# Kernel optimization log

Hardware: AMD Instinct MI355X
Metric: run time of the kernel (lower is better)

Reference implementation:

```python
import jax, jax.numpy as jnp
import numpy as np

B, T, D = 2, 2048, 1024
HD = 128          # head_dim
NH = 16           # num_attention_heads
NKV = 8           # num_key_value_heads
EPS = 1e-6
ROPE_THETA = 1000000.0


def setup_inputs() -> dict:
    key = jax.random.key(0)
    ks = jax.random.split(key, 7)
    s = 0.02
    return {
        "x": jax.random.normal(ks[0], (B, T, D), dtype=jnp.float32),
        "wq": jax.random.normal(ks[1], (D, NH * HD), dtype=jnp.float32) * s,
        "wk": jax.random.normal(ks[2], (D, NKV * HD), dtype=jnp.float32) * s,
        "wv": jax.random.normal(ks[3], (D, NKV * HD), dtype=jnp.float32) * s,
        "wo": jax.random.normal(ks[4], (NH * HD, D), dtype=jnp.float32) * s,
        "q_norm_w": jnp.ones((HD,), dtype=jnp.float32),
        "k_norm_w": jnp.ones((HD,), dtype=jnp.float32),
    }


def _rms_norm(x, w):
    # torch source: x / (rms + eps) * w  (eps added OUTSIDE the sqrt)
    rms = jnp.sqrt(jnp.mean(x * x, axis=-1, keepdims=True))
    return w * (x / (rms + EPS))


def _rope_cos_sin(seq_len):
    pos = jnp.arange(seq_len, dtype=jnp.float32)
    thetas = ROPE_THETA ** (-2.0 * jnp.arange(HD // 2, dtype=jnp.float32) / HD)
    freqs = pos[:, None] * thetas[None, :]            # [T, HD//2]
    return jnp.cos(freqs), jnp.sin(freqs)


def _apply_rope(x, cos, sin):
    # x: [B, H, T, HD]; interleaved complex pairs (view_as_complex layout)
    xr = x[..., 0::2]
    xi = x[..., 1::2]
    c = cos[None, None, :, :]
    s = sin[None, None, :, :]
    out_r = xr * c - xi * s
    out_i = xr * s + xi * c
    return jnp.stack([out_r, out_i], axis=-1).reshape(x.shape)


def reference(x, wq, wk, wv, wo, q_norm_w, k_norm_w):
    b, t, d = x.shape
    q = (x @ wq).reshape(b, t, NH, HD).transpose(0, 2, 1, 3)    # [B,NH,T,HD]
    k = (x @ wk).reshape(b, t, NKV, HD).transpose(0, 2, 1, 3)   # [B,NKV,T,HD]
    v = (x @ wv).reshape(b, t, NKV, HD).transpose(0, 2, 1, 3)

    q = _rms_norm(q, q_norm_w)
    k = _rms_norm(k, k_norm_w)

    rep = NH // NKV
    k = jnp.repeat(k, rep, axis=1)   # GQA expand -> [B,NH,T,HD]
    v = jnp.repeat(v, rep, axis=1)

    cos, sin = _rope_cos_sin(t)
    q = _apply_rope(q, cos, sin)
    k = _apply_rope(k, cos, sin)

    scale = 1.0 / jnp.sqrt(jnp.float32(HD))
    scores = jnp.einsum("bhqd,bhkd->bhqk", q, k) * scale        # [B,NH,T,T]
    mask = jnp.triu(jnp.full((t, t), -jnp.inf, dtype=scores.dtype), k=1)
    scores = scores + mask
    attn = jax.nn.softmax(scores.astype(jnp.float32), axis=-1).astype(q.dtype)
    y = jnp.einsum("bhqk,bhkd->bhqd", attn, v)                  # [B,NH,T,HD]
    y = y.transpose(0, 2, 1, 3).reshape(b, t, NH * HD)
    return y @ wo
```

## Files before the change

### kernel.cpp

```cpp
#include <hip/hip_runtime.h>
#include <hip/hip_bf16.h>
#include <cstdint>
#include <cstddef>

using bf16 = __hip_bfloat16;
using short8 = __attribute__((ext_vector_type(8))) short;
using f32x4  = __attribute__((ext_vector_type(4))) float;
using f32x16 = __attribute__((ext_vector_type(16))) float;

#define DEVI __device__ __forceinline__

DEVI void async_ld16(const void* g, void* l) {
  __builtin_amdgcn_global_load_lds(
      (const __attribute__((address_space(1))) unsigned int*)g,
      (__attribute__((address_space(3))) unsigned int*)l, 16, 0, 0);
}

DEVI unsigned int cvt_pk_bf16(float lo, float hi) {
  unsigned int r;
  asm("v_cvt_pk_bf16_f32 %0, %1, %2" : "=v"(r) : "v"(lo), "v"(hi));
  return r;
}

__global__ __launch_bounds__(256) void prep(
    const float* __restrict__ x, const float* __restrict__ wq,
    const float* __restrict__ wk, const float* __restrict__ wv,
    const float* __restrict__ wo, bf16* __restrict__ xb,
    bf16* __restrict__ wt, bf16* __restrict__ wot, float2* __restrict__ tab) {
  const int z = blockIdx.x, tid = threadIdx.x;
  if (z < 4096) {
    int i = z * 256 + tid;
    float4 v = ((const float4*)x)[i];
    union { bf16 h[4]; ushort4 u; } o;
    o.h[0] = __float2bfloat16(v.x);
    o.h[1] = __float2bfloat16(v.y);
    o.h[2] = __float2bfloat16(v.z);
    o.h[3] = __float2bfloat16(v.w);
    ((ushort4*)xb)[i] = o.u;
  } else if (z < 10240) {
    __shared__ float tile[32][33];
    const float* src; bf16* dst; int N, K, n0, k0, roff;
    if (z < 8192) {
      int z2 = z - 4096;
      int xb_ = z2 & 31, yb = (z2 >> 5) & 31, zz = z2 >> 10;
      if (zz < 2)       { src = wq; N = 2048; n0 = zz * 1024 + xb_ * 32; roff = zz * 1024 + xb_ * 32; }
      else if (zz == 2) { src = wk; N = 1024; n0 = xb_ * 32; roff = 2048 + xb_ * 32; }
      else              { src = wv; N = 1024; n0 = xb_ * 32; roff = 3072 + xb_ * 32; }
      K = 1024; k0 = yb * 32; dst = wt;
    } else {
      int z3 = z - 8192;
      int xb_ = z3 & 31, yb = z3 >> 5;
      src = wo; N = 1024; K = 2048; n0 = xb_ * 32; k0 = yb * 32; roff = xb_ * 32;
      dst = wot;
    }
    int tx = tid & 31, ty = tid >> 5;
#pragma unroll
    for (int i = 0; i < 32; i += 8)
      tile[ty + i][tx] = src[(size_t)(k0 + ty + i) * N + n0 + tx];
    __syncthreads();
#pragma unroll
    for (int i = 0; i < 32; i += 8)
      dst[(size_t)(roff + ty + i) * K + k0 + tx] = __float2bfloat16(tile[tx][ty + i]);
  } else {
    int z4 = z - 10240;
    int t = z4 * 4 + (tid >> 6), i = tid & 63;
    float ex = -2.f * (float)i * (1.f / 128.f);
    float theta = exp2f(ex * 19.9315685693241741f);
    float f = (float)t * theta;
    float sv, cv;
    sincosf(f, &sv, &cv);
    tab[t * 64 + i] = make_float2(cv, sv);
  }
}

__global__ __launch_bounds__(256, 2) void gemm_qkv(
    const bf16* __restrict__ A, const bf16* __restrict__ Bt,
    const float* __restrict__ qnw, const float* __restrict__ knw,
    const float2* __restrict__ tab,
    bf16* __restrict__ Qh, bf16* __restrict__ Kh, bf16* __restrict__ Vt) {
  __shared__ alignas(16) bf16 As[2][128 * 64];
  __shared__ alignas(16) bf16 Bs[2][128 * 64];
  const int tid = threadIdx.x, lane = tid & 63, w = tid >> 6;
  const int wm = w >> 1, wn = w & 1;
  const int bx = blockIdx.x;
  const int m0 = blockIdx.y * 128, n0 = bx * 128;
  const int K = 1024, nt = 16;
  f32x4 acc[4][4] = {};

  const int srow = lane >> 3;
  const int scb  = (lane & 7) * 16;

  auto stage = [&](int buf, int kt) {
#pragma unroll
    for (int i = 0; i < 4; i++) {
      int row = w * 32 + i * 8 + srow;
      int src_cb = scb ^ ((row & 7) << 4);
      async_ld16((const char*)(A  + (size_t)(m0 + row) * K + kt * 64) + src_cb,
                 (char*)As[buf] + w * 4096 + i * 1024);
      async_ld16((const char*)(Bt + (size_t)(n0 + row) * K + kt * 64) + src_cb,
                 (char*)Bs[buf] + w * 4096 + i * 1024);
    }
  };

  stage(0, 0);
  stage(1, 1);

  for (int kt = 0; kt < nt; ++kt) {
    const int buf = kt & 1;
    if (kt + 1 < nt) asm volatile("s_waitcnt vmcnt(8)" ::: "memory");
    else             asm volatile("s_waitcnt vmcnt(0)" ::: "memory");
    __builtin_amdgcn_s_barrier();
#pragma unroll
    for (int ks = 0; ks < 2; ks++) {
      short8 af[4], bfr[4];
#pragma unroll
      for (int mi = 0; mi < 4; mi++) {
        int row = wm * 64 + mi * 16 + (lane & 15);
        int cb = (ks * 64 + (lane >> 4) * 16) ^ ((row & 7) << 4);
        af[mi] = *(const short8*)((const char*)As[buf] + row * 128 + cb);
      }
#pragma unroll
      for (int ni = 0; ni < 4; ni++) {
        int row = wn * 64 + ni * 16 + (lane & 15);
        int cb = (ks * 64 + (lane >> 4) * 16) ^ ((row & 7) << 4);
        bfr[ni] = *(const short8*)((const char*)Bs[buf] + row * 128 + cb);
      }
#pragma unroll
      for (int mi = 0; mi < 4; mi++)
#pragma unroll
        for (int ni = 0; ni < 4; ni++)
          acc[mi][ni] = __builtin_amdgcn_mfma_f32_16x16x32_bf16(af[mi], bfr[ni], acc[mi][ni], 0, 0, 0);
    }
    __builtin_amdgcn_s_barrier();
    __builtin_amdgcn_sched_barrier(0);
    if (kt + 2 < nt) stage(buf, kt + 2);
  }

  const int b = m0 >> 11;

  if (bx < 24) {
    __syncthreads();
    float* ssb = (float*)As;
    float s[4][4];
#pragma unroll
    for (int mi = 0; mi < 4; mi++)
#pragma unroll
      for (int r = 0; r < 4; r++) {
        float v0 = acc[mi][0][r], v1 = acc[mi][1][r];
        float v2 = acc[mi][2][r], v3 = acc[mi][3][r];
        float t = v0 * v0 + v1 * v1 + v2 * v2 + v3 * v3;
        t += __shfl_xor(t, 1);
        t += __shfl_xor(t, 2);
        t += __shfl_xor(t, 4);
        t += __shfl_xor(t, 8);
        s[mi][r] = t;
      }
    if ((lane & 15) == 0) {
#pragma unroll
      for (int mi = 0; mi < 4; mi++)
#pragma unroll
        for (int r = 0; r < 4; r++)
          ssb[wn * 128 + wm * 64 + mi * 16 + (lane >> 4) * 4 + r] = s[mi][r];
    }
    __syncthreads();

    const int isQ = (bx < 16);
    const int h = isQ ? bx : bx - 16;
    const float* wnp = isQ ? qnw : knw;
    bf16* dst = isQ ? Qh : Kh;
    const int NHH = isQ ? 16 : 8;
    const float qs = isQ ? 0.12751744416163417f : 1.f;
    float wd[4];
#pragma unroll
    for (int ni = 0; ni < 4; ni++) wd[ni] = wnp[wn * 64 + ni * 16 + (lane & 15)];

#pragma unroll
    for (int mi = 0; mi < 4; mi++)
#pragma unroll
      for (int r = 0; r < 4; r++) {
        int rl = wm * 64 + mi * 16 + (lane >> 4) * 4 + r;
        float tot = ssb[rl] + ssb[128 + rl];
        float inv = qs / (sqrtf(tot * 0.0078125f) + 1e-6f);
        int t = (m0 + rl) & 2047;
        bf16* drow = dst + ((size_t)(b * NHH + h) * 2048 + t) * 128;
#pragma unroll
        for (int ni = 0; ni < 4; ni++) {
          int d = wn * 64 + ni * 16 + (lane & 15);
          float val = acc[mi][ni][r] * inv * wd[ni];
          float prt = __shfl_xor(val, 1);
          float2 cs = tab[t * 64 + (d >> 1)];
          float o = (d & 1) ? (prt * cs.y + val * cs.x)
                            : (val * cs.x - prt * cs.y);
          drow[d] = __float2bfloat16(o);
        }
      }
  } else {
    __syncthreads();
    bf16* vt = (bf16*)As;
    const int vh = bx - 24;
#pragma unroll
    for (int mi = 0; mi < 4; mi++)
#pragma unroll
      for (int ni = 0; ni < 4; ni++) {
        int d = wn * 64 + ni * 16 + (lane & 15);
        int tl = wm * 64 + mi * 16 + (lane >> 4) * 4;
        unsigned int p0 = cvt_pk_bf16(acc[mi][ni][0], acc[mi][ni][1]);
        unsigned int p1 = cvt_pk_bf16(acc[mi][ni][2], acc[mi][ni][3]);
        int byte = d * 256 + ((tl * 2) ^ ((d & 7) << 4));
        *(uint2*)((char*)vt + byte) = make_uint2(p0, p1);
      }
    __syncthreads();
    bf16* dstV = Vt + (size_t)(b * 8 + vh) * 128 * 2048 + (m0 & 2047);
#pragma unroll
    for (int i = 0; i < 8; i++) {
      int flat = tid + i * 256;
      int d = flat >> 4, g = flat & 15;
      short8 v = *(const short8*)((const char*)vt + d * 256 + ((g * 16) ^ ((d & 7) << 4)));
      *(short8*)(dstV + (size_t)d * 2048 + g * 8) = v;
    }
  }
}

__global__ __launch_bounds__(256, 3) void gemm_out64(
    const bf16* __restrict__ A, const bf16* __restrict__ Bt,
    float* __restrict__ C, int M, int N, int K) {
  __shared__ alignas(16) bf16 As[2][64 * 64];
  __shared__ alignas(16) bf16 Bs[2][128 * 64];
  const int tid = threadIdx.x, lane = tid & 63, w = tid >> 6;
  const int m0 = blockIdx.y * 64, n0 = blockIdx.x * 128;
  const int nt = K >> 6;
  f32x4 acc[4][2] = {};

  auto stage = [&](int buf, int kt) {
#pragma unroll
    for (int i = 0; i < 2; i++) {
      int c = tid + i * 256;
      int row = c >> 3;
      int cb = ((c & 7) * 16) ^ ((row & 7) << 4);
      async_ld16((const char*)(A + (size_t)(m0 + row) * K + kt * 64) + cb,
                 (char*)As[buf] + i * 4096 + tid * 16);
    }
#pragma unroll
    for (int i = 0; i < 4; i++) {
      int c = tid + i * 256;
      int row = c >> 3;
      int cb = ((c & 7) * 16) ^ ((row & 7) << 4);
      async_ld16((const char*)(Bt + (size_t)(n0 + row) * K + kt * 64) + cb,
                 (char*)Bs[buf] + i * 4096 + tid * 16);
    }
  };

  stage(0, 0);
  stage(1, 1);

  for (int kt = 0; kt < nt; ++kt) {
    const int buf = kt & 1;
    if (kt + 1 < nt) asm volatile("s_waitcnt vmcnt(6)" ::: "memory");
    else             asm volatile("s_waitcnt vmcnt(0)" ::: "memory");
    __builtin_amdgcn_s_barrier();
#pragma unroll
    for (int ks = 0; ks < 2; ks++) {
      short8 af[4], bfr[2];
#pragma unroll
      for (int mi = 0; mi < 4; mi++) {
        int row = mi * 16 + (lane & 15);
        int cb = (ks * 64 + (lane >> 4) * 16) ^ ((row & 7) << 4);
        af[mi] = *(const short8*)((const char*)As[buf] + row * 128 + cb);
      }
#pragma unroll
      for (int ni = 0; ni < 2; ni++) {
        int row = w * 32 + ni * 16 + (lane & 15);
        int cb = (ks * 64 + (lane >> 4) * 16) ^ ((row & 7) << 4);
        bfr[ni] = *(const short8*)((const char*)Bs[buf] + row * 128 + cb);
      }
#pragma unroll
      for (int mi = 0; mi < 4; mi++)
#pragma unroll
        for (int ni = 0; ni < 2; ni++)
          acc[mi][ni] = __builtin_amdgcn_mfma_f32_16x16x32_bf16(af[mi], bfr[ni], acc[mi][ni], 0, 0, 0);
    }
    __builtin_amdgcn_s_barrier();
    __builtin_amdgcn_sched_barrier(0);
    if (kt + 2 < nt) stage(buf, kt + 2);
  }

  const int c0 = n0 + w * 32 + (lane & 15);
  const int r0 = m0 + (lane >> 4) * 4;
#pragma unroll
  for (int mi = 0; mi < 4; mi++)
#pragma unroll
    for (int ni = 0; ni < 2; ni++)
#pragma unroll
      for (int r = 0; r < 4; r++)
        C[(size_t)(r0 + mi * 16 + r) * N + (c0 + ni * 16)] = acc[mi][ni][r];
}

__global__ __launch_bounds__(512, 1) void flash_attn10(
    const bf16* __restrict__ Qh, const bf16* __restrict__ Kh,
    const bf16* __restrict__ Vt, bf16* __restrict__ Y) {
  __shared__ alignas(16) bf16 KB[4][64 * 128];
  __shared__ alignas(16) bf16 VB[4][128 * 64];
  __shared__ float MLs[128][2];
  const int tid = threadIdx.x, lane = tid & 63, w = tid >> 6;
  const int hi = lane >> 5, lq = lane & 31;
  const int grp = w >> 2, wl = w & 3;

  const int g = blockIdx.x;
  const int bh = (g & 7) * 4 + ((g >> 3) & 3);
  const int p  = g >> 5;
  const int b = bh >> 4, h = bh & 15, kvh = h >> 1;

  const bf16* Qg = Qh + (size_t)(b * 16 + h) * 2048 * 128;
  const bf16* Kg = Kh + (size_t)(b * 8 + kvh) * 2048 * 128;
  const bf16* Vg = Vt + (size_t)(b * 8 + kvh) * 128 * 2048;

  short8 qf[8];
  f32x16 oacc[4];
  float m, l;
  int qw = 0, qg = 0;

  auto stage2 = [&](int set, int k0e) {
#pragma unroll
    for (int gb = 0; gb < 2; gb++) {
      const int k0 = k0e + gb * 64;
      char* kb = (char*)KB[set * 2 + gb];
      char* vb = (char*)VB[set * 2 + gb];
#pragma unroll
      for (int i = 0; i < 2; i++) {
        int c = w * 2 + i;
        {
          int row = c * 4 + (lane >> 4);
          int cb = ((lane & 15) * 16) ^ ((row & 7) << 4);
          async_ld16((const char*)Kg + (size_t)(k0 + row) * 256 + cb, kb + c * 1024);
        }
        {
          int row = c * 8 + (lane >> 3);
          int cb = ((lane & 7) * 16) ^ ((row & 7) << 4);
          async_ld16((const char*)Vg + (size_t)row * 4096 + (size_t)k0 * 2 + cb, vb + c * 1024);
        }
      }
    }
  };

  auto setupTile = [&](int q0) {
    qw = q0 + wl * 32;
    qg = qw + lq;
#pragma unroll
    for (int dc = 0; dc < 8; dc++)
      qf[dc] = *(const short8*)(Qg + (size_t)qg * 128 + dc * 16 + hi * 8);
#pragma unroll
    for (int dc = 0; dc < 4; dc++)
#pragma unroll
      for (int r = 0; r < 16; r++) oacc[dc][r] = 0.f;
    m = -1e30f;
    l = 0.f;
  };

  auto computeStep = [&](int bufI, int k0) {
    f32x16 st[2] = {};
#pragma unroll
    for (int kc = 0; kc < 2; kc++) {
      int row = kc * 32 + lq;
      int swz = (row & 7) << 4;
      const char* kbase = (const char*)KB[bufI] + row * 256;
#pragma unroll
      for (int dc = 0; dc < 8; dc++) {
        short8 kf = *(const short8*)(kbase + ((dc * 32 + hi * 16) ^ swz));
        st[kc] = __builtin_amdgcn_mfma_f32_32x32x16_bf16(kf, qf[dc], st[kc], 0, 0, 0);
      }
    }
    const bool msk = (k0 + 63 > qw);
    if (msk) {
#pragma unroll
      for (int kc = 0; kc < 2; kc++)
#pragma unroll
        for (int rr = 0; rr < 16; rr++) {
          int kg = k0 + kc * 32 + (rr & 3) + 8 * (rr >> 2) + 4 * hi;
          if (kg > qg) st[kc][rr] = -1e30f;
        }
    }
    float mx[16];
#pragma unroll
    for (int rr = 0; rr < 16; rr++) mx[rr] = fmaxf(st[0][rr], st[1][rr]);
#pragma unroll
    for (int off = 8; off >= 1; off >>= 1)
#pragma unroll
      for (int rr = 0; rr < 8; rr++)
        if (rr < off) mx[rr] = fmaxf(mx[rr], mx[rr + off]);
    float pm = fmaxf(mx[0], __shfl_xor(mx[0], 32));
    if (__any(pm > m + 8.f)) {
      float mnew = fmaxf(m, pm);
      float alpha = exp2f(m - mnew);
      m = mnew;
      l *= alpha;
      float al[16];
#pragma unroll
      for (int rr = 0; rr < 16; rr++)
        al[rr] = __shfl(alpha, (rr & 3) + 8 * (rr >> 2) + 4 * hi);
#pragma unroll
      for (int dc = 0; dc < 4; dc++)
#pragma unroll
        for (int rr = 0; rr < 16; rr++) oacc[dc][rr] *= al[rr];
    }
#pragma unroll
    for (int kc = 0; kc < 2; kc++)
#pragma unroll
      for (int rr = 0; rr < 16; rr++) st[kc][rr] = exp2f(st[kc][rr] - m);
    float sm[16];
#pragma unroll
    for (int rr = 0; rr < 16; rr++) sm[rr] = st[0][rr] + st[1][rr];
#pragma unroll
    for (int off = 8; off >= 1; off >>= 1)
#pragma unroll
      for (int rr = 0; rr < 8; rr++)
        if (rr < off) sm[rr] += sm[rr + off];
    l += sm[0] + __shfl_xor(sm[0], 32);
    short8 af[4];
#pragma unroll
    for (int kc = 0; kc < 2; kc++)
#pragma unroll
      for (int sb = 0; sb < 2; sb++) {
        int base = sb * 8;
        unsigned int a01 = cvt_pk_bf16(st[kc][base + 0], st[kc][base + 1]);
        unsigned int a23 = cvt_pk_bf16(st[kc][base + 2], st[kc][base + 3]);
        unsigned int b01 = cvt_pk_bf16(st[kc][base + 4], st[kc][base + 5]);
        unsigned int b23 = cvt_pk_bf16(st[kc][base + 6], st[kc][base + 7]);
        unsigned int xa01 = (unsigned int)__shfl_xor((int)a01, 32);
        unsigned int xa23 = (unsigned int)__shfl_xor((int)a23, 32);
        unsigned int xb01 = (unsigned int)__shfl_xor((int)b01, 32);
        unsigned int xb23 = (unsigned int)__shfl_xor((int)b23, 32);
        union { unsigned int u[4]; short8 s; } f;
        f.u[0] = hi ? xb01 : a01;
        f.u[1] = hi ? xb23 : a23;
        f.u[2] = hi ? b01 : xa01;
        f.u[3] = hi ? b23 : xa23;
        af[kc * 2 + sb] = f.s;
      }
#pragma unroll
    for (int dc = 0; dc < 4; dc++) {
      int row = dc * 32 + lq;
      int swz = (row & 7) << 4;
      const char* vbase = (const char*)VB[bufI] + row * 128;
#pragma unroll
      for (int ks = 0; ks < 4; ks++) {
        short8 vf = *(const short8*)(vbase + ((ks * 32 + hi * 16) ^ swz));
        oacc[dc] = __builtin_amdgcn_mfma_f32_32x32x16_bf16(af[ks], vf, oacc[dc], 0, 0, 0);
      }
    }
  };

  auto runRounds = [&](int n) {
    const int R = n >> 1;
    for (int r = 0; r < R; ++r) {
      asm volatile("s_waitcnt vmcnt(0)" ::: "memory");
      __builtin_amdgcn_s_barrier();
      if (r + 1 < R) stage2((r + 1) & 1, (2 * r + 2) * 64);
      __builtin_amdgcn_sched_barrier(0);
      const int s = 2 * r + grp, k0 = s * 64;
      const int bufI = (r & 1) * 2 + grp;
      if (k0 < qw + 32) computeStep(bufI, k0);
    }
  };

  auto writePartials = [&]() {
    float* base = (wl < 2) ? (float*)KB[2] : (float*)VB[2];
#pragma unroll
    for (int dc = 0; dc < 4; dc++)
#pragma unroll
      for (int rr = 0; rr < 16; rr++) {
        int q = (wl & 1) * 32 + (rr & 3) + 8 * (rr >> 2) + 4 * hi;
        base[q * 128 + dc * 32 + lq] = oacc[dc][rr];
      }
    if (lane < 32) {
      MLs[wl * 32 + lane][0] = m;
      MLs[wl * 32 + lane][1] = l;
    }
  };

  auto mergeAndY = [&](int q0) {
    float m1 = MLs[wl * 32 + lq][0], l1 = MLs[wl * 32 + lq][1];
    float mN = fmaxf(m, m1);
    float e0 = exp2f(m - mN), e1 = exp2f(m1 - mN);
    float lT = l * e0 + l1 * e1;
    float inv = 1.f / lT;
    float e0r[16], e1r[16], ivr[16];
#pragma unroll
    for (int rr = 0; rr < 16; rr++) {
      int src = (rr & 3) + 8 * (rr >> 2) + 4 * hi;
      e0r[rr] = __shfl(e0, src);
      e1r[rr] = __shfl(e1, src);
      ivr[rr] = __shfl(inv, src);
    }
    const float* base = (wl < 2) ? (const float*)KB[2] : (const float*)VB[2];
#pragma unroll
    for (int dc = 0; dc < 4; dc++)
#pragma unroll
      for (int rr = 0; rr < 16; rr++) {
        int q = (wl & 1) * 32 + (rr & 3) + 8 * (rr >> 2) + 4 * hi;
        float o1 = base[q * 128 + dc * 32 + lq];
        float oT = oacc[dc][rr] * e0r[rr] + o1 * e1r[rr];
        int t = q0 + wl * 32 + (rr & 3) + 8 * (rr >> 2) + 4 * hi;
        Y[(size_t)(b * 2048 + t) * 2048 + h * 128 + dc * 32 + lq] =
            __float2bfloat16(oT * ivr[rr]);
      }
  };

  const int jA = 15 - p, jB = p;
  const int q0A = jA * 128, nA = 2 * jA + 2;
  const int q0B = jB * 128, nB = 2 * jB + 2;

  setupTile(q0A);
  stage2(0, 0);
  runRounds(nA);
  __syncthreads();
  stage2(0, 0);
  if (grp == 1) writePartials();
  __syncthreads();
  if (grp == 0) mergeAndY(q0A);
  setupTile(q0B);
  runRounds(nB);
  __syncthreads();
  if (grp == 1) writePartials();
  __syncthreads();
  if (grp == 0) mergeAndY(q0B);
}

extern "C" void kernel_launch(void* const* d_in, const int* in_sizes, int n_in,
                              void* d_out, int out_size, void* d_ws, size_t ws_size,
                              hipStream_t stream) {
  (void)in_sizes; (void)n_in; (void)out_size; (void)ws_size;
  const float* x   = (const float*)d_in[0];
  const float* wq  = (const float*)d_in[1];
  const float* wk  = (const float*)d_in[2];
  const float* wv  = (const float*)d_in[3];
  const float* wo  = (const float*)d_in[4];
  const float* qnw = (const float*)d_in[5];
  const float* knw = (const float*)d_in[6];
  float* out = (float*)d_out;
  char* ws = (char*)d_ws;
  const size_t MB = 1u << 20;
  bf16*   xb  = (bf16*)(ws + 0 * MB);
  bf16*   wt  = (bf16*)(ws + 8 * MB);
  bf16*   wot = (bf16*)(ws + 16 * MB);
  float2* tab = (float2*)(ws + 52 * MB);
  bf16*   Qh  = (bf16*)(ws + 53 * MB);
  bf16*   Kh  = (bf16*)(ws + 69 * MB);
  bf16*   Vtr = (bf16*)(ws + 77 * MB);
  bf16*   Yb  = (bf16*)(ws + 85 * MB);

  prep<<<10752, 256, 0, stream>>>(x, wq, wk, wv, wo, xb, wt, wot, tab);
  gemm_qkv<<<dim3(32, 32), 256, 0, stream>>>(xb, wt, qnw, knw, tab, Qh, Kh, Vtr);
  flash_attn10<<<256, 512, 0, stream>>>(Qh, Kh, Vtr, Yb);
  gemm_out64<<<dim3(8, 64), 256, 0, stream>>>(Yb, wot, out, 4096, 1024, 2048);
}
```

Measured before the change: 156.2 us.

## Shrink flash-attention blocks to 256 threads with 64-row Q tiles, two blocks per CU

The attention kernel moves from 512-thread blocks covering 128 query rows to 256-thread blocks covering 64 query rows, with KV steps of 32 keys. The grid doubles to 512 blocks and launch bounds allow two blocks per CU. LDS is repacked into one ~66KB buffer, and the K/V staging swizzle and V fragment indexing are rewritten for the smaller tiles. The aim is better occupancy and latency hiding, at the cost of more online-softmax bookkeeping per key and more merge passes.

```diff
diff --git a/kernel.cpp b/kernel.cpp
--- a/kernel.cpp
+++ b/kernel.cpp
@@ -295,15 +295,13 @@
         C[(size_t)(r0 + mi * 16 + r) * N + (c0 + ni * 16)] = acc[mi][ni][r];
 }
 
-__global__ __launch_bounds__(512, 1) void flash_attn10(
+__global__ __launch_bounds__(256, 2) void flash_attn11(
     const bf16* __restrict__ Qh, const bf16* __restrict__ Kh,
     const bf16* __restrict__ Vt, bf16* __restrict__ Y) {
-  __shared__ alignas(16) bf16 KB[4][64 * 128];
-  __shared__ alignas(16) bf16 VB[4][128 * 64];
-  __shared__ float MLs[128][2];
+  __shared__ alignas(16) char SMEM[66048];
   const int tid = threadIdx.x, lane = tid & 63, w = tid >> 6;
   const int hi = lane >> 5, lq = lane & 31;
-  const int grp = w >> 2, wl = w & 3;
+  const int grp = w >> 1, wl = w & 1;
 
   const int g = blockIdx.x;
   const int bh = (g & 7) * 4 + ((g >> 3) & 3);
@@ -314,6 +312,9 @@
   const bf16* Kg = Kh + (size_t)(b * 8 + kvh) * 2048 * 128;
   const bf16* Vg = Vt + (size_t)(b * 8 + kvh) * 128 * 2048;
 
+  float* scratch = (float*)SMEM;
+  float* MLs = (float*)(SMEM + 65536);
+
   short8 qf[8];
   f32x16 oacc[4];
   float m, l;
@@ -322,21 +323,24 @@
   auto stage2 = [&](int set, int k0e) {
 #pragma unroll
     for (int gb = 0; gb < 2; gb++) {
-      const int k0 = k0e + gb * 64;
-      char* kb = (char*)KB[set * 2 + gb];
-      char* vb = (char*)VB[set * 2 + gb];
+      const int k0 = k0e + gb * 32;
+      char* kb = SMEM + (set * 2 + gb) * 8192;
+      char* vb = SMEM + 32768 + (set * 2 + gb) * 8192;
 #pragma unroll
       for (int i = 0; i < 2; i++) {
-        int c = w * 2 + i;
+        int c = tid + i * 256;
         {
-          int row = c * 4 + (lane >> 4);
-          int cb = ((lane & 15) * 16) ^ ((row & 7) << 4);
-          async_ld16((const char*)Kg + (size_t)(k0 + row) * 256 + cb, kb + c * 1024);
+          int row = c >> 4, slot = c & 15;
+          async_ld16((const char*)Kg + (size_t)(k0 + row) * 256 +
+                         ((slot * 16) ^ ((row & 15) << 4)),
+                     kb + c * 16);
         }
         {
-          int row = c * 8 + (lane >> 3);
-          int cb = ((lane & 7) * 16) ^ ((row & 7) << 4);
-          async_ld16((const char*)Vg + (size_t)row * 4096 + (size_t)k0 * 2 + cb, vb + c * 1024);
+          int row = c >> 3, slot = c & 7;
+          int lg = slot ^ (row & 7);
+          int d = row * 2 + (lg >> 2);
+          async_ld16((const char*)Vg + (size_t)d * 4096 + (size_t)k0 * 2 + (lg & 3) * 16,
+                     vb + c * 16);
         }
       }
     }
@@ -357,35 +361,28 @@
   };
 
   auto computeStep = [&](int bufI, int k0) {
-    f32x16 st[2] = {};
-#pragma unroll
-    for (int kc = 0; kc < 2; kc++) {
-      int row = kc * 32 + lq;
-      int swz = (row & 7) << 4;
-      const char* kbase = (const char*)KB[bufI] + row * 256;
-#pragma unroll
-      for (int dc = 0; dc < 8; dc++) {
-        short8 kf = *(const short8*)(kbase + ((dc * 32 + hi * 16) ^ swz));
-        st[kc] = __builtin_amdgcn_mfma_f32_32x32x16_bf16(kf, qf[dc], st[kc], 0, 0, 0);
-      }
-    }
-    const bool msk = (k0 + 63 > qw);
-    if (msk) {
-#pragma unroll
-      for (int kc = 0; kc < 2; kc++)
-#pragma unroll
-        for (int rr = 0; rr < 16; rr++) {
-          int kg = k0 + kc * 32 + (rr & 3) + 8 * (rr >> 2) + 4 * hi;
-          if (kg > qg) st[kc][rr] = -1e30f;
-        }
-    }
-    float mx[16];
-#pragma unroll
-    for (int rr = 0; rr < 16; rr++) mx[rr] = fmaxf(st[0][rr], st[1][rr]);
-#pragma unroll
-    for (int off = 8; off >= 1; off >>= 1)
-#pragma unroll
-      for (int rr = 0; rr < 8; rr++)
+    f32x16 st = {};
+    const char* kbase = SMEM + bufI * 8192 + lq * 256;
+    const int kswz = (lq & 15) << 4;
+#pragma unroll
+    for (int dc = 0; dc < 8; dc++) {
+      short8 kf = *(const short8*)(kbase + ((dc * 32 + hi * 16) ^ kswz));
+      st = __builtin_amdgcn_mfma_f32_32x32x16_bf16(kf, qf[dc], st, 0, 0, 0);
+    }
+    if (k0 + 31 > qw) {
+#pragma unroll
+      for (int rr = 0; rr < 16; rr++) {
+        int kg = k0 + (rr & 3) + 8 * (rr >> 2) + 4 * hi;
+        if (kg > qg) st[rr] = -1e30f;
+      }
+    }
+    float mx[8];
+#pragma unroll
+    for (int rr = 0; rr < 8; rr++) mx[rr] = fmaxf(st[rr], st[rr + 8]);
+#pragma unroll
+    for (int off = 4; off >= 1; off >>= 1)
+#pragma unroll
+      for (int rr = 0; rr < 4; rr++)
         if (rr < off) mx[rr] = fmaxf(mx[rr], mx[rr + off]);
     float pm = fmaxf(mx[0], __shfl_xor(mx[0], 32));
     if (__any(pm > m + 8.f)) {
@@ -403,82 +400,77 @@
         for (int rr = 0; rr < 16; rr++) oacc[dc][rr] *= al[rr];
     }
 #pragma unroll
-    for (int kc = 0; kc < 2; kc++)
-#pragma unroll
-      for (int rr = 0; rr < 16; rr++) st[kc][rr] = exp2f(st[kc][rr] - m);
-    float sm[16];
-#pragma unroll
-    for (int rr = 0; rr < 16; rr++) sm[rr] = st[0][rr] + st[1][rr];
-#pragma unroll
-    for (int off = 8; off >= 1; off >>= 1)
-#pragma unroll
-      for (int rr = 0; rr < 8; rr++)
+    for (int rr = 0; rr < 16; rr++) st[rr] = exp2f(st[rr] - m);
+    float sm[8];
+#pragma unroll
+    for (int rr = 0; rr < 8; rr++) sm[rr] = st[rr] + st[rr + 8];
+#pragma unroll
+    for (int off = 4; off >= 1; off >>= 1)
+#pragma unroll
+      for (int rr = 0; rr < 4; rr++)
         if (rr < off) sm[rr] += sm[rr + off];
     l += sm[0] + __shfl_xor(sm[0], 32);
-    short8 af[4];
-#pragma unroll
-    for (int kc = 0; kc < 2; kc++)
-#pragma unroll
-      for (int sb = 0; sb < 2; sb++) {
-        int base = sb * 8;
-        unsigned int a01 = cvt_pk_bf16(st[kc][base + 0], st[kc][base + 1]);
-        unsigned int a23 = cvt_pk_bf16(st[kc][base + 2], st[kc][base + 3]);
-        unsigned int b01 = cvt_pk_bf16(st[kc][base + 4], st[kc][base + 5]);
-        unsigned int b23 = cvt_pk_bf16(st[kc][base + 6], st[kc][base + 7]);
-        unsigned int xa01 = (unsigned int)__shfl_xor((int)a01, 32);
-        unsigned int xa23 = (unsigned int)__shfl_xor((int)a23, 32);
-        unsigned int xb01 = (unsigned int)__shfl_xor((int)b01, 32);
-        unsigned int xb23 = (unsigned int)__shfl_xor((int)b23, 32);
-        union { unsigned int u[4]; short8 s; } f;
-        f.u[0] = hi ? xb01 : a01;
-        f.u[1] = hi ? xb23 : a23;
-        f.u[2] = hi ? b01 : xa01;
-        f.u[3] = hi ? b23 : xa23;
-        af[kc * 2 + sb] = f.s;
-      }
+    short8 af[2];
+#pragma unroll
+    for (int sb = 0; sb < 2; sb++) {
+      int base = sb * 8;
+      unsigned int a01 = cvt_pk_bf16(st[base + 0], st[base + 1]);
+      unsigned int a23 = cvt_pk_bf16(st[base + 2], st[base + 3]);
+      unsigned int b01 = cvt_pk_bf16(st[base + 4], st[base + 5]);
+      unsigned int b23 = cvt_pk_bf16(st[base + 6], st[base + 7]);
+      unsigned int xa01 = (unsigned int)__shfl_xor((int)a01, 32);
+      unsigned int xa23 = (unsigned int)__shfl_xor((int)a23, 32);
+      unsigned int xb01 = (unsigned int)__shfl_xor((int)b01, 32);
+      unsigned int xb23 = (unsigned int)__shfl_xor((int)b23, 32);
+      union { unsigned int u[4]; short8 s; } f;
+      f.u[0] = hi ? xb01 : a01;
+      f.u[1] = hi ? xb23 : a23;
+      f.u[2] = hi ? b01 : xa01;
+      f.u[3] = hi ? b23 : xa23;
+      af[sb] = f.s;
+    }
+    const char* vbB = SMEM + 32768 + bufI * 8192;
 #pragma unroll
     for (int dc = 0; dc < 4; dc++) {
-      int row = dc * 32 + lq;
-      int swz = (row & 7) << 4;
-      const char* vbase = (const char*)VB[bufI] + row * 128;
-#pragma unroll
-      for (int ks = 0; ks < 4; ks++) {
-        short8 vf = *(const short8*)(vbase + ((ks * 32 + hi * 16) ^ swz));
+      int vrow = dc * 16 + (lq >> 1);
+      int vswz = (vrow & 7) << 4;
+      const char* vbase = vbB + vrow * 128;
+#pragma unroll
+      for (int ks = 0; ks < 2; ks++) {
+        short8 vf = *(const short8*)(vbase + (((lq & 1) * 64 + ks * 32 + hi * 16) ^ vswz));
         oacc[dc] = __builtin_amdgcn_mfma_f32_32x32x16_bf16(af[ks], vf, oacc[dc], 0, 0, 0);
       }
     }
   };
 
-  auto runRounds = [&](int n) {
-    const int R = n >> 1;
+  auto runRounds = [&](int R) {
     for (int r = 0; r < R; ++r) {
       asm volatile("s_waitcnt vmcnt(0)" ::: "memory");
       __builtin_amdgcn_s_barrier();
-      if (r + 1 < R) stage2((r + 1) & 1, (2 * r + 2) * 64);
+      if (r + 1 < R) stage2((r + 1) & 1, (r + 1) * 64);
       __builtin_amdgcn_sched_barrier(0);
-      const int s = 2 * r + grp, k0 = s * 64;
+      const int k0 = (2 * r + grp) * 32;
       const int bufI = (r & 1) * 2 + grp;
       if (k0 < qw + 32) computeStep(bufI, k0);
     }
   };
 
   auto writePartials = [&]() {
-    float* base = (wl < 2) ? (float*)KB[2] : (float*)VB[2];
 #pragma unroll
     for (int dc = 0; dc < 4; dc++)
 #pragma unroll
       for (int rr = 0; rr < 16; rr++) {
-        int q = (wl & 1) * 32 + (rr & 3) + 8 * (rr >> 2) + 4 * hi;
-        base[q * 128 + dc * 32 + lq] = oacc[dc][rr];
+        int q = wl * 32 + (rr & 3) + 8 * (rr >> 2) + 4 * hi;
+        scratch[q * 128 + dc * 32 + lq] = oacc[dc][rr];
       }
     if (lane < 32) {
-      MLs[wl * 32 + lane][0] = m;
-      MLs[wl * 32 + lane][1] = l;
+      MLs[(wl * 32 + lane) * 2] = m;
+      MLs[(wl * 32 + lane) * 2 + 1] = l;
     }
   };
 
   auto mergeAndY = [&](int q0) {
-    float m1 = MLs[wl * 32 + lq][0], l1 = MLs[wl * 32 + lq][1];
+    float m1 = MLs[(wl * 32 + lq) * 2], l1 = MLs[(wl * 32 + lq) * 2 + 1];
     float mN = fmaxf(m, m1);
     float e0 = exp2f(m - mN), e1 = exp2f(m1 - mN);
     float lT = l * e0 + l1 * e1;
@@ -491,34 +483,33 @@
       e1r[rr] = __shfl(e1, src);
       ivr[rr] = __shfl(inv, src);
     }
-    const float* base = (wl < 2) ? (const float*)KB[2] : (const float*)VB[2];
 #pragma unroll
     for (int dc = 0; dc < 4; dc++)
 #pragma unroll
       for (int rr = 0; rr < 16; rr++) {
-        int q = (wl & 1) * 32 + (rr & 3) + 8 * (rr >> 2) + 4 * hi;
-        float o1 = base[q * 128 + dc * 32 + lq];
+        int q = wl * 32 + (rr & 3) + 8 * (rr >> 2) + 4 * hi;
+        float o1 = scratch[q * 128 + dc * 32 + lq];
         float oT = oacc[dc][rr] * e0r[rr] + o1 * e1r[rr];
-        int t = q0 + wl * 32 + (rr & 3) + 8 * (rr >> 2) + 4 * hi;
+        int t = q0 + q;
         Y[(size_t)(b * 2048 + t) * 2048 + h * 128 + dc * 32 + lq] =
             __float2bfloat16(oT * ivr[rr]);
       }
   };
 
-  const int jA = 15 - p, jB = p;
-  const int q0A = jA * 128, nA = 2 * jA + 2;
-  const int q0B = jB * 128, nB = 2 * jB + 2;
+  const int jA = 31 - p, jB = p;
+  const int q0A = jA * 64, q0B = jB * 64;
 
   setupTile(q0A);
   stage2(0, 0);
-  runRounds(nA);
+  runRounds(jA + 1);
   __syncthreads();
-  stage2(0, 0);
   if (grp == 1) writePartials();
   __syncthreads();
   if (grp == 0) mergeAndY(q0A);
+  __syncthreads();
   setupTile(q0B);
-  runRounds(nB);
+  stage2(0, 0);
+  runRounds(jB + 1);
   __syncthreads();
   if (grp == 1) writePartials();
   __syncthreads();
@@ -550,6 +541,6 @@
 
   prep<<<10752, 256, 0, stream>>>(x, wq, wk, wv, wo, xb, wt, wot, tab);
   gemm_qkv<<<dim3(32, 32), 256, 0, stream>>>(xb, wt, qnw, knw, tab, Qh, Kh, Vtr);
-  flash_attn10<<<256, 512, 0, stream>>>(Qh, Kh, Vtr, Yb);
+  flash_attn11<<<512, 256, 0, stream>>>(Qh, Kh, Vtr, Yb);
   gemm_out64<<<dim3(8, 64), 256, 0, stream>>>(Yb, wot, out, 4096, 1024, 2048);
 }
```

New measurement: 161.2 us. 3.2% more time.

## Halve QKV GEMM K-tile to 32 with paired-row swizzle for higher occupancy

Applied to the files above, without the earlier changes.

The QKV projection GEMM now stages 32-wide K slices instead of 64, which cuts its shared memory from 64KB to 32KB, and the launch bound now asks for 4 blocks per CU instead of 2. A new LDS layout packs two rows per 128-byte line with an XOR swizzle so fragment reads avoid bank conflicts. The aim is higher occupancy, so more blocks hide load latency. In exchange there are twice as many K iterations, each with a barrier, and the 4-blocks bound may limit registers for the 64-float accumulator.

```diff
diff --git a/kernel.cpp b/kernel.cpp
--- a/kernel.cpp
+++ b/kernel.cpp
@@ -73,32 +73,31 @@
   }
 }
 
-__global__ __launch_bounds__(256, 2) void gemm_qkv(
+__global__ __launch_bounds__(256, 4) void gemm_qkv32(
     const bf16* __restrict__ A, const bf16* __restrict__ Bt,
     const float* __restrict__ qnw, const float* __restrict__ knw,
     const float2* __restrict__ tab,
     bf16* __restrict__ Qh, bf16* __restrict__ Kh, bf16* __restrict__ Vt) {
-  __shared__ alignas(16) bf16 As[2][128 * 64];
-  __shared__ alignas(16) bf16 Bs[2][128 * 64];
+  __shared__ alignas(16) char SMEM[32768];
   const int tid = threadIdx.x, lane = tid & 63, w = tid >> 6;
   const int wm = w >> 1, wn = w & 1;
   const int bx = blockIdx.x;
   const int m0 = blockIdx.y * 128, n0 = bx * 128;
-  const int K = 1024, nt = 16;
+  const int K = 1024, nt = 32;
   f32x4 acc[4][4] = {};
 
-  const int srow = lane >> 3;
-  const int scb  = (lane & 7) * 16;
-
   auto stage = [&](int buf, int kt) {
 #pragma unroll
-    for (int i = 0; i < 4; i++) {
-      int row = w * 32 + i * 8 + srow;
-      int src_cb = scb ^ ((row & 7) << 4);
-      async_ld16((const char*)(A  + (size_t)(m0 + row) * K + kt * 64) + src_cb,
-                 (char*)As[buf] + w * 4096 + i * 1024);
-      async_ld16((const char*)(Bt + (size_t)(n0 + row) * K + kt * 64) + src_cb,
-                 (char*)Bs[buf] + w * 4096 + i * 1024);
+    for (int i = 0; i < 2; i++) {
+      int c = tid + i * 256;
+      int pi = c >> 3;
+      int s  = (c & 7) ^ (pi & 7);
+      int row = pi * 2 + (s >> 2);
+      int sb  = (s & 3) * 16;
+      async_ld16((const char*)(A  + (size_t)(m0 + row) * K + kt * 32) + sb,
+                 SMEM + buf * 8192 + c * 16);
+      async_ld16((const char*)(Bt + (size_t)(n0 + row) * K + kt * 32) + sb,
+                 SMEM + 16384 + buf * 8192 + c * 16);
     }
   };
 
@@ -107,30 +106,33 @@
 
   for (int kt = 0; kt < nt; ++kt) {
     const int buf = kt & 1;
-    if (kt + 1 < nt) asm volatile("s_waitcnt vmcnt(8)" ::: "memory");
+    if (kt + 1 < nt) asm volatile("s_waitcnt vmcnt(4)" ::: "memory");
     else             asm volatile("s_waitcnt vmcnt(0)" ::: "memory");
     __builtin_amdgcn_s_barrier();
-#pragma unroll
-    for (int ks = 0; ks < 2; ks++) {
-      short8 af[4], bfr[4];
-#pragma unroll
-      for (int mi = 0; mi < 4; mi++) {
-        int row = wm * 64 + mi * 16 + (lane & 15);
-        int cb = (ks * 64 + (lane >> 4) * 16) ^ ((row & 7) << 4);
-        af[mi] = *(const short8*)((const char*)As[buf] + row * 128 + cb);
-      }
-#pragma unroll
-      for (int ni = 0; ni < 4; ni++) {
-        int row = wn * 64 + ni * 16 + (lane & 15);
-        int cb = (ks * 64 + (lane >> 4) * 16) ^ ((row & 7) << 4);
-        bfr[ni] = *(const short8*)((const char*)Bs[buf] + row * 128 + cb);
-      }
-#pragma unroll
-      for (int mi = 0; mi < 4; mi++)
-#pragma unroll
-        for (int ni = 0; ni < 4; ni++)
-          acc[mi][ni] = __builtin_amdgcn_mfma_f32_16x16x32_bf16(af[mi], bfr[ni], acc[mi][ni], 0, 0, 0);
-    }
+
+    const char* Ab = SMEM + buf * 8192;
+    const char* Bb = SMEM + 16384 + buf * 8192;
+    short8 af[4], bfr[4];
+#pragma unroll
+    for (int mi = 0; mi < 4; mi++) {
+      int r = wm * 64 + mi * 16 + (lane & 15);
+      int pi = r >> 1;
+      int sl = (((r & 1) << 2) + (lane >> 4)) ^ (pi & 7);
+      af[mi] = *(const short8*)(Ab + pi * 128 + sl * 16);
+    }
+#pragma unroll
+    for (int ni = 0; ni < 4; ni++) {
+      int r = wn * 64 + ni * 16 + (lane & 15);
+      int pi = r >> 1;
+      int sl = (((r & 1) << 2) + (lane >> 4)) ^ (pi & 7);
+      bfr[ni] = *(const short8*)(Bb + pi * 128 + sl * 16);
+    }
+#pragma unroll
+    for (int mi = 0; mi < 4; mi++)
+#pragma unroll
+      for (int ni = 0; ni < 4; ni++)
+        acc[mi][ni] = __builtin_amdgcn_mfma_f32_16x16x32_bf16(af[mi], bfr[ni], acc[mi][ni], 0, 0, 0);
+
     __builtin_amdgcn_s_barrier();
     __builtin_amdgcn_sched_barrier(0);
     if (kt + 2 < nt) stage(buf, kt + 2);
@@ -140,7 +142,7 @@
 
   if (bx < 24) {
     __syncthreads();
-    float* ssb = (float*)As;
+    float* ssb = (float*)SMEM;
     float s[4][4];
 #pragma unroll
     for (int mi = 0; mi < 4; mi++)
@@ -196,7 +198,7 @@
       }
   } else {
     __syncthreads();
-    bf16* vt = (bf16*)As;
+    bf16* vt = (bf16*)SMEM;
     const int vh = bx - 24;
 #pragma unroll
     for (int mi = 0; mi < 4; mi++)
@@ -549,7 +551,7 @@
   bf16*   Yb  = (bf16*)(ws + 85 * MB);
 
   prep<<<10752, 256, 0, stream>>>(x, wq, wk, wv, wo, xb, wt, wot, tab);
-  gemm_qkv<<<dim3(32, 32), 256, 0, stream>>>(xb, wt, qnw, knw, tab, Qh, Kh, Vtr);
+  gemm_qkv32<<<dim3(32, 32), 256, 0, stream>>>(xb, wt, qnw, knw, tab, Qh, Kh, Vtr);
   flash_attn10<<<256, 512, 0, stream>>>(Qh, Kh, Vtr, Yb);
   gemm_out64<<<dim3(8, 64), 256, 0, stream>>>(Yb, wot, out, 4096, 1024, 2048);
 }
```

Result: no change. 157.2 us (+0.7%).
